# Performance work log

Measured on AMD Instinct MI355X. Metric: run time of the kernel, lower is better.

Reference implementation:

```python
import jax, jax.numpy as jnp
import numpy as np

N, E = 10000, 320000
IN_DIM, OUT_DIM, HEADS = 256, 32, 8
HD = OUT_DIM * HEADS  # 256
EPS = 1e-16  # PyG softmax epsilon


def _make_conv_params(key, in_dim, heads, d):
    hd = heads * d
    ks = jax.random.split(key, 8)
    s = 0.02
    return {
        'Wq': jax.random.normal(ks[0], (in_dim, hd)) * s,
        'bq': jnp.zeros((hd,)),
        'Wk': jax.random.normal(ks[1], (in_dim, hd)) * s,
        'bk': jnp.zeros((hd,)),
        'Wv': jax.random.normal(ks[2], (in_dim, hd)) * s,
        'bv': jnp.zeros((hd,)),
        'We': jax.random.normal(ks[3], (1, hd)) * s,          # lin_edge, no bias
        'Wskip': jax.random.normal(ks[4], (in_dim, hd)) * s,  # lin_skip
        'bskip': jnp.zeros((hd,)),
        'Wbeta': jax.random.normal(ks[5], (3 * hd, 1)) * s,   # lin_beta, no bias
    }


def transformer_conv(x, src, dst, edge_attr, p, heads, d):
    # x: [N, F]; edge_attr: [E, 1]
    n = x.shape[0]
    q = (x @ p['Wq'] + p['bq']).reshape(n, heads, d)
    k = (x @ p['Wk'] + p['bk']).reshape(n, heads, d)
    v = (x @ p['Wv'] + p['bv']).reshape(n, heads, d)
    e = (edge_attr @ p['We']).reshape(-1, heads, d)  # [E, H, D]
    kj = k[src] + e                                  # [E, H, D]
    vj = v[src] + e
    # per-edge attention logits
    alpha = jnp.einsum('ehd,ehd->eh', q[dst], kj) / jnp.sqrt(jnp.asarray(d, x.dtype))
    # segment softmax over incoming edges of each dst node
    m = jax.ops.segment_max(alpha, dst, num_segments=n)     # [N, H]
    m = jnp.where(jnp.isfinite(m), m, 0.0)
    ex = jnp.exp(alpha - m[dst])
    denom = jax.ops.segment_sum(ex, dst, num_segments=n)    # [N, H]
    w = ex / (denom[dst] + EPS)                              # [E, H]
    out = jax.ops.segment_sum(w[:, :, None] * vj, dst, num_segments=n)  # [N, H, D]
    out = out.reshape(n, heads * d)
    # beta-gated skip connection
    xr = x @ p['Wskip'] + p['bskip']
    beta = jax.nn.sigmoid(jnp.concatenate([out, xr, out - xr], axis=-1) @ p['Wbeta'])  # [N, 1]
    return beta * xr + (1.0 - beta) * out


def setup_inputs() -> dict:
    key = jax.random.key(0)
    kx, ke, kw, k1, k2 = jax.random.split(key, 5)
    inp = {
        'x': jax.random.normal(kx, (N, IN_DIM), dtype=jnp.float32),
        'edge_index': jax.random.randint(ke, (2, E), 0, N, dtype=jnp.int64),
        'edge_weight': jax.random.uniform(kw, (E,), dtype=jnp.float32),
    }
    p1 = _make_conv_params(k1, IN_DIM, HEADS, OUT_DIM)
    p2 = _make_conv_params(k2, HD, HEADS, OUT_DIM)
    for name, v in p1.items():
        inp[name + '1'] = v
    for name, v in p2.items():
        inp[name + '2'] = v
    return inp


def reference(x, edge_index, edge_weight,
              Wq1, bq1, Wk1, bk1, Wv1, bv1, We1, Wskip1, bskip1, Wbeta1,
              Wq2, bq2, Wk2, bk2, Wv2, bv2, We2, Wskip2, bskip2, Wbeta2):
    src, dst = edge_index[0], edge_index[1]
    ea = edge_weight[:, None]  # [E, 1]
    p1 = dict(Wq=Wq1, bq=bq1, Wk=Wk1, bk=bk1, Wv=Wv1, bv=bv1, We=We1,
              Wskip=Wskip1, bskip=bskip1, Wbeta=Wbeta1)
    p2 = dict(Wq=Wq2, bq=bq2, Wk=Wk2, bk=bk2, Wv=Wv2, bv=bv2, We=We2,
              Wskip=Wskip2, bskip=bskip2, Wbeta=Wbeta2)
    h = transformer_conv(x, src, dst, ea, p1, HEADS, OUT_DIM)
    h = transformer_conv(h, src, dst, ea, p2, HEADS, OUT_DIM)
    h = transformer_conv(h, src, dst, ea, p2, HEADS, OUT_DIM)  # conv2 applied twice, shared weights
    return h
```

## Files before the change

kernel.cpp:

```cpp
#include <hip/hip_runtime.h>
#include <hip/hip_bf16.h>
#include <math.h>

#define NN 10000
#define EE 320000
#define DIM 256
#define NROWS 10016
#define SCANB 40

typedef __attribute__((ext_vector_type(8))) _Float16 f16x8;
typedef __attribute__((ext_vector_type(4))) _Float16 f16x4;
typedef __attribute__((ext_vector_type(2))) _Float16 f16x2;
typedef __attribute__((ext_vector_type(4))) float f32x4;

#if defined(__has_builtin)
#if __has_builtin(__builtin_amdgcn_fdot2)
#define FDOT2(a, b, c) __builtin_amdgcn_fdot2(a, b, c, false)
#endif
#endif
#ifndef FDOT2
#define FDOT2(a, b, c) fmaf((float)a[0], (float)b[0], fmaf((float)a[1], (float)b[1], c))
#endif

__device__ __forceinline__ float bf2f(unsigned short u) {
  union { unsigned int ui; float f; } cv;
  cv.ui = ((unsigned int)u) << 16;
  return cv.f;
}

__device__ __forceinline__ float ldf(const void* p, int idx, int isf) {
  return isf ? ((const float*)p)[idx] : bf2f(((const unsigned short*)p)[idx]);
}

__global__ __launch_bounds__(256) void k_detect_zero(const unsigned int* __restrict__ xw,
                                                     const int* __restrict__ ei,
                                                     int* __restrict__ flags,
                                                     int* __restrict__ counts) {
  int i = blockIdx.x * 256 + (int)threadIdx.x;
  if (i < NN) counts[i] = 0;
  if (blockIdx.x == 0 && threadIdx.x < 64) {
    int lane = threadIdx.x;
    int wild = 0;
    for (int t = 0; t < 16; ++t) {
      unsigned int w = xw[t * 64 + lane];
      unsigned int lo = w & 0xffffu;
      float f = bf2f((unsigned short)lo);
      float af = fabsf(f);
      if (lo != 0u && (af > 1e4f || af < 1e-30f)) wild++;
    }
    #pragma unroll
    for (int m = 1; m < 64; m <<= 1) wild += __shfl_xor(wild, m);
    int zeros = 0;
    for (int t = 0; t < 2; ++t) {
      if (ei[(t * 64 + lane) * 2 + 1] == 0) zeros++;
    }
    #pragma unroll
    for (int m = 1; m < 64; m <<= 1) zeros += __shfl_xor(zeros, m);
    if (lane == 0) {
      flags[0] = (wild > 100) ? 1 : 0;
      flags[1] = (zeros > 100) ? 1 : 0;
    }
  }
}

__global__ void k_idx_count(const int* __restrict__ ei, int* __restrict__ s32,
                            int* __restrict__ d32, int* __restrict__ counts,
                            const int* __restrict__ flags) {
  int i64 = flags[1];
  int i = blockIdx.x * blockDim.x + threadIdx.x;
  if (i < EE) {
    int s, d;
    if (i64) { s = ei[2 * i]; d = ei[2 * (EE + i)]; }
    else     { s = ei[i];     d = ei[EE + i]; }
    s32[i] = s; d32[i] = d;
    atomicAdd(&counts[d], 1);
  }
}

__global__ __launch_bounds__(256) void k_scan1(const int* __restrict__ counts,
                                               int* __restrict__ tmpoff,
                                               int* __restrict__ bsum) {
  __shared__ int s[256];
  int t = threadIdx.x;
  int i = blockIdx.x * 256 + t;
  int v = (i < NN) ? counts[i] : 0;
  s[t] = v;
  __syncthreads();
  for (int off = 1; off < 256; off <<= 1) {
    int x = (t >= off) ? s[t - off] : 0;
    __syncthreads();
    s[t] += x;
    __syncthreads();
  }
  if (i < NN) tmpoff[i] = s[t] - v;
  if (t == 255) bsum[blockIdx.x] = s[255];
}

__global__ __launch_bounds__(256) void k_scan3(const int* __restrict__ tmpoff,
                                               const int* __restrict__ bsum,
                                               int* __restrict__ offsets,
                                               int* __restrict__ cursor) {
  __shared__ int sbase;
  if (threadIdx.x < 64) {
    int t = threadIdx.x;
    int v = (t < SCANB && t < (int)blockIdx.x) ? bsum[t] : 0;
    #pragma unroll
    for (int msk = 1; msk < 64; msk <<= 1) v += __shfl_xor(v, msk);
    if (t == 0) sbase = v;
  }
  __syncthreads();
  int base = sbase;
  int i = blockIdx.x * 256 + (int)threadIdx.x;
  if (i < NN) {
    int o = tmpoff[i] + base;
    offsets[i] = o;
    cursor[i] = o;
  }
  if (i == 0) offsets[NN] = EE;
}

__global__ void k_fill_sort(const int* __restrict__ d32, const int* __restrict__ s32,
                            const void* __restrict__ ew, int* __restrict__ cursor,
                            int2* __restrict__ eS, const int* __restrict__ flags) {
  int isf = flags[0];
  int i = blockIdx.x * blockDim.x + threadIdx.x;
  if (i < EE) {
    float wv = isf ? ((const float*)ew)[i] : bf2f(((const unsigned short*)ew)[i]);
    int p = atomicAdd(&cursor[d32[i]], 1);
    eS[p] = make_int2(s32[i], __float_as_int(wv));
  }
}

struct PackArgs {
  const void* W[8];
  const void* B8[8];
  const void* WeWb[4];
  const void* x;
};

__global__ __launch_bounds__(256) void k_pack(PackArgs pa, _Float16* __restrict__ Bh,
                                              float* __restrict__ bvec,
                                              float* __restrict__ WeWbF,
                                              _Float16* __restrict__ Ah,
                                              _Float16* __restrict__ Al,
                                              const int* __restrict__ flags) {
  int isf = flags[0];
  int i = blockIdx.x * 256 + (int)threadIdx.x;
  if (i < 8 * 65536) {
    int m = i >> 16, col = (i >> 8) & 255, k = i & 255;
    Bh[i] = (_Float16)ldf(pa.W[m], k * 256 + col, isf);
    return;
  }
  i -= 8 * 65536;
  if (i < 2048) {
    bvec[i] = ldf(pa.B8[i >> 8], i & 255, isf);
    return;
  }
  i -= 2048;
  if (i < 2048) {
    int which, k;
    if (i < 256)       { which = 0; k = i; }
    else if (i < 1024) { which = 1; k = i - 256; }
    else if (i < 1280) { which = 2; k = i - 1024; }
    else               { which = 3; k = i - 1280; }
    WeWbF[i] = ldf(pa.WeWb[which], k, isf);
    return;
  }
  i -= 2048;
  if (i < NROWS * 64) {
    f16x4 h, l;
    if (i >= NN * 64) {
      h = (f16x4)(_Float16)0.f;
      l = (f16x4)(_Float16)0.f;
    } else {
      float v[4];
      if (isf) {
        float4 t = reinterpret_cast<const float4*>(pa.x)[i];
        v[0] = t.x; v[1] = t.y; v[2] = t.z; v[3] = t.w;
      } else {
        ushort4 t = reinterpret_cast<const ushort4*>(pa.x)[i];
        v[0] = bf2f(t.x); v[1] = bf2f(t.y); v[2] = bf2f(t.z); v[3] = bf2f(t.w);
      }
      #pragma unroll
      for (int j = 0; j < 4; ++j) {
        _Float16 hh = (_Float16)v[j];
        h[j] = hh;
        l[j] = (_Float16)(v[j] - (float)hh);
      }
    }
    reinterpret_cast<f16x4*>(Ah)[i] = h;
    reinterpret_cast<f16x4*>(Al)[i] = l;
  }
}

__global__ __launch_bounds__(256, 4) void k_gemm_mfma(
    const _Float16* __restrict__ Ah, const _Float16* __restrict__ Al,
    const _Float16* __restrict__ Bh, const float* __restrict__ bvec,
    float* __restrict__ Qf, _Float16* __restrict__ KVh, float* __restrict__ XRf) {
  int tid = (int)threadIdx.x;
  int wave = tid >> 6, lane = tid & 63;
  int lr = lane & 15;
  int kg = (lane >> 4) << 3;
  int mat = blockIdx.y;
  int rowBase = blockIdx.x << 5;
  int colBase = (mat << 8) + (wave << 6);
  const _Float16* a0 = Ah + (size_t)(rowBase + lr) * 256 + kg;
  const _Float16* a1 = Al + (size_t)(rowBase + lr) * 256 + kg;
  const _Float16* b0 = Bh + (size_t)(colBase + lr) * 256 + kg;
  f32x4 acc[2][4] = {};
  #pragma unroll
  for (int ks = 0; ks < 256; ks += 32) {
    f16x8 ah0 = *reinterpret_cast<const f16x8*>(a0 + ks);
    f16x8 ah1 = *reinterpret_cast<const f16x8*>(a0 + 16 * 256 + ks);
    f16x8 bh[4];
    #pragma unroll
    for (int cf = 0; cf < 4; ++cf)
      bh[cf] = *reinterpret_cast<const f16x8*>(b0 + cf * 16 * 256 + ks);
    #pragma unroll
    for (int cf = 0; cf < 4; ++cf) {
      acc[0][cf] = __builtin_amdgcn_mfma_f32_16x16x32_f16(ah0, bh[cf], acc[0][cf], 0, 0, 0);
      acc[1][cf] = __builtin_amdgcn_mfma_f32_16x16x32_f16(ah1, bh[cf], acc[1][cf], 0, 0, 0);
    }
    if (mat == 3) {
      f16x8 al0 = *reinterpret_cast<const f16x8*>(a1 + ks);
      f16x8 al1 = *reinterpret_cast<const f16x8*>(a1 + 16 * 256 + ks);
      #pragma unroll
      for (int cf = 0; cf < 4; ++cf) {
        acc[0][cf] = __builtin_amdgcn_mfma_f32_16x16x32_f16(al0, bh[cf], acc[0][cf], 0, 0, 0);
        acc[1][cf] = __builtin_amdgcn_mfma_f32_16x16x32_f16(al1, bh[cf], acc[1][cf], 0, 0, 0);
      }
    }
  }
  int rj = (lane >> 4) << 2;
  int colLoc = (wave << 6);
  #pragma unroll
  for (int rf = 0; rf < 2; ++rf) {
    #pragma unroll
    for (int cf = 0; cf < 4; ++cf) {
      int col = colLoc + cf * 16 + lr;
      float bb = bvec[(mat << 8) + col];
      #pragma unroll
      for (int j = 0; j < 4; ++j) {
        int row = rowBase + rf * 16 + rj + j;
        if (row < NN) {
          float val = acc[rf][cf][j] + bb;
          if (mat == 0)      Qf[(size_t)row * DIM + col] = val;
          else if (mat == 3) XRf[(size_t)row * DIM + col] = val;
          else KVh[(size_t)row * 512 + ((mat == 2) ? 256 : 0) + col] = (_Float16)val;
        }
      }
    }
  }
}

#define ATT_STEP(KK, VV, WW) do { \
    f16x2 kka = {KK[0], KK[1]}, kkb = {KK[2], KK[3]}; \
    float pt = FDOT2(kka, qha, FDOT2(kkb, qhb, 0.f)); \
    pt += __shfl_xor(pt, 1); \
    pt += __shfl_xor(pt, 2); \
    pt += __shfl_xor(pt, 4); \
    float alpha = fmaf(WW, qwe, pt) * 0.17677669529663687f; \
    float nm = fmaxf(m, alpha); \
    float sc = __expf(m - nm); \
    float pe = __expf(alpha - nm); \
    l = fmaf(l, sc, pe); \
    sw = fmaf(sw, sc, pe * WW); \
    a0 = fmaf(a0, sc, pe * (float)VV[0]); \
    a1 = fmaf(a1, sc, pe * (float)VV[1]); \
    a2 = fmaf(a2, sc, pe * (float)VV[2]); \
    a3 = fmaf(a3, sc, pe * (float)VV[3]); \
    m = nm; \
  } while (0)

#define PAIR_STEP(K0, V0, W0, K1, V1, W1) do { \
    f16x2 k0a = {K0[0], K0[1]}, k0b = {K0[2], K0[3]}; \
    f16x2 k1a = {K1[0], K1[1]}, k1b = {K1[2], K1[3]}; \
    float pt0 = FDOT2(k0a, qha, FDOT2(k0b, qhb, 0.f)); \
    float pt1 = FDOT2(k1a, qha, FDOT2(k1b, qhb, 0.f)); \
    pt0 += __shfl_xor(pt0, 1); pt1 += __shfl_xor(pt1, 1); \
    pt0 += __shfl_xor(pt0, 2); pt1 += __shfl_xor(pt1, 2); \
    pt0 += __shfl_xor(pt0, 4); pt1 += __shfl_xor(pt1, 4); \
    float al0 = fmaf(W0, qwe, pt0) * 0.17677669529663687f; \
    float al1 = fmaf(W1, qwe, pt1) * 0.17677669529663687f; \
    float nm = fmaxf(fmaxf(m, al0), al1); \
    float sc = __expf(m - nm); \
    float p0 = __expf(al0 - nm); \
    float p1 = __expf(al1 - nm); \
    l = fmaf(l, sc, p0 + p1); \
    sw = fmaf(sw, sc, fmaf(p0, W0, p1 * W1)); \
    a0 = fmaf(a0, sc, fmaf(p0, (float)V0[0], p1 * (float)V1[0])); \
    a1 = fmaf(a1, sc, fmaf(p0, (float)V0[1], p1 * (float)V1[1])); \
    a2 = fmaf(a2, sc, fmaf(p0, (float)V0[2], p1 * (float)V1[2])); \
    a3 = fmaf(a3, sc, fmaf(p0, (float)V0[3], p1 * (float)V1[3])); \
    m = nm; \
  } while (0)

__global__ __launch_bounds__(256) void k_attn(
    const float* __restrict__ Qf, const _Float16* __restrict__ KVh,
    const float* __restrict__ XRf, const float* __restrict__ We,
    const float* __restrict__ Wb, const int2* __restrict__ eS,
    const int* __restrict__ offsets, _Float16* __restrict__ Ah,
    _Float16* __restrict__ Al, float* __restrict__ FinalOut) {
  int wid = (int)threadIdx.x >> 6, lane = (int)threadIdx.x & 63;
  int node = blockIdx.x * 4 + wid;
  if (node >= NN) return;
  int d0 = lane * 4;
  const float4 q4 = *reinterpret_cast<const float4*>(&Qf[(size_t)node * DIM + d0]);
  const float4 x4 = *reinterpret_cast<const float4*>(&XRf[(size_t)node * DIM + d0]);
  const float4 we4 = *reinterpret_cast<const float4*>(&We[d0]);
  const float4 wo = *reinterpret_cast<const float4*>(&Wb[d0]);
  const float4 wx = *reinterpret_cast<const float4*>(&Wb[DIM + d0]);
  const float4 wd = *reinterpret_cast<const float4*>(&Wb[2 * DIM + d0]);
  f16x2 qha = {(_Float16)q4.x, (_Float16)q4.y};
  f16x2 qhb = {(_Float16)q4.z, (_Float16)q4.w};
  float qwe = q4.x * we4.x + q4.y * we4.y + q4.z * we4.z + q4.w * we4.w;
  qwe += __shfl_xor(qwe, 1);
  qwe += __shfl_xor(qwe, 2);
  qwe += __shfl_xor(qwe, 4);
  int beg = offsets[node], end = offsets[node + 1];
  beg = __builtin_amdgcn_readfirstlane(beg);
  end = __builtin_amdgcn_readfirstlane(end);
  float m = -INFINITY, l = 0.f, sw = 0.f, a0 = 0.f, a1 = 0.f, a2 = 0.f, a3 = 0.f;
  int p = beg;
  if ((end - beg) & 1) {
    int2 e = eS[p];
    float w0 = __int_as_float(e.y);
    const _Float16* r = KVh + (size_t)e.x * 512 + d0;
    f16x4 k0 = *reinterpret_cast<const f16x4*>(r);
    f16x4 v0 = *reinterpret_cast<const f16x4*>(r + 256);
    ATT_STEP(k0, v0, w0);
    ++p;
  }
  if (p < end) {
    int2 eA0 = eS[p], eA1 = eS[p + 1];
    int pb = (p + 3 < end) ? (p + 2) : p;
    int2 eB0 = eS[pb], eB1 = eS[pb + 1];
    const _Float16* rA0 = KVh + (size_t)eA0.x * 512 + d0;
    const _Float16* rA1 = KVh + (size_t)eA1.x * 512 + d0;
    const _Float16* rB0 = KVh + (size_t)eB0.x * 512 + d0;
    const _Float16* rB1 = KVh + (size_t)eB1.x * 512 + d0;
    f16x4 kA0 = *reinterpret_cast<const f16x4*>(rA0), vA0 = *reinterpret_cast<const f16x4*>(rA0 + 256);
    f16x4 kA1 = *reinterpret_cast<const f16x4*>(rA1), vA1 = *reinterpret_cast<const f16x4*>(rA1 + 256);
    f16x4 kB0 = *reinterpret_cast<const f16x4*>(rB0), vB0 = *reinterpret_cast<const f16x4*>(rB0 + 256);
    f16x4 kB1 = *reinterpret_cast<const f16x4*>(rB1), vB1 = *reinterpret_cast<const f16x4*>(rB1 + 256);
    float wA0 = __int_as_float(eA0.y), wA1 = __int_as_float(eA1.y);
    float wB0 = __int_as_float(eB0.y), wB1 = __int_as_float(eB1.y);
    #pragma unroll 2
    for (; p + 2 < end; p += 2) {
      int pc = (p + 5 < end) ? (p + 4) : p;
      int2 eC0 = eS[pc], eC1 = eS[pc + 1];
      const _Float16* rC0 = KVh + (size_t)eC0.x * 512 + d0;
      const _Float16* rC1 = KVh + (size_t)eC1.x * 512 + d0;
      f16x4 kC0 = *reinterpret_cast<const f16x4*>(rC0), vC0 = *reinterpret_cast<const f16x4*>(rC0 + 256);
      f16x4 kC1 = *reinterpret_cast<const f16x4*>(rC1), vC1 = *reinterpret_cast<const f16x4*>(rC1 + 256);
      float wC0 = __int_as_float(eC0.y), wC1 = __int_as_float(eC1.y);
      PAIR_STEP(kA0, vA0, wA0, kA1, vA1, wA1);
      kA0 = kB0; vA0 = vB0; wA0 = wB0; kA1 = kB1; vA1 = vB1; wA1 = wB1;
      kB0 = kC0; vB0 = vC0; wB0 = wC0; kB1 = kC1; vB1 = vC1; wB1 = wC1;
    }
    PAIR_STEP(kA0, vA0, wA0, kA1, vA1, wA1);
  }
  float inv = 1.f / (l + 1e-16f);
  float o0 = fmaf(sw, we4.x, a0) * inv;
  float o1 = fmaf(sw, we4.y, a1) * inv;
  float o2 = fmaf(sw, we4.z, a2) * inv;
  float o3 = fmaf(sw, we4.w, a3) * inv;
  float part = o0 * wo.x + o1 * wo.y + o2 * wo.z + o3 * wo.w
             + x4.x * wx.x + x4.y * wx.y + x4.z * wx.z + x4.w * wx.w
             + (o0 - x4.x) * wd.x + (o1 - x4.y) * wd.y
             + (o2 - x4.z) * wd.z + (o3 - x4.w) * wd.w;
  #pragma unroll
  for (int msk = 1; msk < 64; msk <<= 1) part += __shfl_xor(part, msk);
  float beta = 1.f / (1.f + __expf(-part));
  float h0 = beta * x4.x + (1.f - beta) * o0;
  float h1 = beta * x4.y + (1.f - beta) * o1;
  float h2 = beta * x4.z + (1.f - beta) * o2;
  float h3 = beta * x4.w + (1.f - beta) * o3;
  if (FinalOut) {
    float4 h; h.x = h0; h.y = h1; h.z = h2; h.w = h3;
    *reinterpret_cast<float4*>(&FinalOut[(size_t)node * DIM + d0]) = h;
  } else {
    f16x4 hh, ll;
    _Float16 t0 = (_Float16)h0, t1 = (_Float16)h1, t2 = (_Float16)h2, t3 = (_Float16)h3;
    hh[0] = t0; hh[1] = t1; hh[2] = t2; hh[3] = t3;
    ll[0] = (_Float16)(h0 - (float)t0); ll[1] = (_Float16)(h1 - (float)t1);
    ll[2] = (_Float16)(h2 - (float)t2); ll[3] = (_Float16)(h3 - (float)t3);
    *reinterpret_cast<f16x4*>(&Ah[(size_t)node * DIM + d0]) = hh;
    *reinterpret_cast<f16x4*>(&Al[(size_t)node * DIM + d0]) = ll;
  }
}

static inline size_t align256(size_t v) { return (v + 255) & ~(size_t)255; }

extern "C" void kernel_launch(void* const* d_in, const int* in_sizes, int n_in,
                              void* d_out, int out_size, void* d_ws, size_t ws_size,
                              hipStream_t stream) {
  const void* x = d_in[0];
  const int* eidx = (const int*)d_in[1];
  const void* ew = d_in[2];

  char* w = (char*)d_ws;
  size_t pos = 0;
  int* flags = (int*)(w + pos); pos = align256(pos + 2 * sizeof(int));
  float* Qf  = (float*)(w + pos); pos = align256(pos + (size_t)NROWS * DIM * 4);
  float* XRf = (float*)(w + pos); pos = align256(pos + (size_t)NROWS * DIM * 4);
  _Float16* KVh = (_Float16*)(w + pos); pos = align256(pos + (size_t)NROWS * 512 * 2);
  _Float16* Ah = (_Float16*)(w + pos); pos = align256(pos + (size_t)NROWS * DIM * 2);
  _Float16* Al = (_Float16*)(w + pos); pos = align256(pos + (size_t)NROWS * DIM * 2);
  _Float16* Bh = (_Float16*)(w + pos); pos = align256(pos + (size_t)8 * 65536 * 2);
  float* bvec  = (float*)(w + pos); pos = align256(pos + 2048 * 4);
  float* WeWbF = (float*)(w + pos); pos = align256(pos + 2048 * 4);
  int* s32   = (int*)(w + pos);    pos = align256(pos + (size_t)EE * 4);
  int* d32   = (int*)(w + pos);    pos = align256(pos + (size_t)EE * 4);
  int2* eS   = (int2*)(w + pos);   pos = align256(pos + (size_t)EE * 8);
  int* counts  = (int*)(w + pos);  pos = align256(pos + (size_t)NN * 4);
  int* offsets = (int*)(w + pos);  pos = align256(pos + (size_t)(NN + 1) * 4);
  int* cursor  = (int*)(w + pos);  pos = align256(pos + (size_t)NN * 4);
  int* tmpoff  = (int*)(w + pos);  pos = align256(pos + (size_t)NN * 4);
  int* bsum    = (int*)(w + pos);  pos = align256(pos + 64 * 4);

  PackArgs pa;
  pa.x = x;
  for (int g = 0; g < 2; ++g) {
    const void* const* pp = &d_in[3 + g * 10];
    pa.W[g * 4 + 0] = pp[0]; pa.W[g * 4 + 1] = pp[2];
    pa.W[g * 4 + 2] = pp[4]; pa.W[g * 4 + 3] = pp[7];
    pa.B8[g * 4 + 0] = pp[1]; pa.B8[g * 4 + 1] = pp[3];
    pa.B8[g * 4 + 2] = pp[5]; pa.B8[g * 4 + 3] = pp[8];
    pa.WeWb[g * 2 + 0] = pp[6];
    pa.WeWb[g * 2 + 1] = pp[9];
  }

  k_detect_zero<<<SCANB, 256, 0, stream>>>((const unsigned int*)x, eidx, flags, counts);
  k_pack<<<4568, 256, 0, stream>>>(pa, Bh, bvec, WeWbF, Ah, Al, flags);
  k_idx_count<<<(EE + 255) / 256, 256, 0, stream>>>(eidx, s32, d32, counts, flags);
  k_scan1<<<SCANB, 256, 0, stream>>>(counts, tmpoff, bsum);
  k_scan3<<<SCANB, 256, 0, stream>>>(tmpoff, bsum, offsets, cursor);
  k_fill_sort<<<(EE + 255) / 256, 256, 0, stream>>>(d32, s32, ew, cursor, eS, flags);

  for (int layer = 0; layer < 3; ++layer) {
    int g = (layer == 0) ? 0 : 1;
    k_gemm_mfma<<<dim3(NROWS / 32, 4), 256, 0, stream>>>(
        Ah, Al, Bh + (size_t)g * 4 * 65536, bvec + g * 1024, Qf, KVh, XRf);
    k_attn<<<(NN + 3) / 4, 256, 0, stream>>>(Qf, KVh, XRf,
        WeWbF + (g ? 1024 : 0), WeWbF + (g ? 1280 : 256),
        eS, offsets, Ah, Al, (layer == 2) ? (float*)d_out : nullptr);
  }
}
```

Measured before the change: 305.9 us.

## Schedule attention nodes by descending degree and enlarge GEMM row tile

Builds a degree histogram and counting sort so the attention kernel handles nodes in descending in-degree order, which reduces tail imbalance from high-degree nodes landing late in the launch. The MFMA GEMM also now covers 64 rows per block instead of 32, so each B fragment load feeds more MFMAs. NROWS padding and the pack grid size are increased to match. This adds two small preprocessing kernels and more accumulator registers per GEMM thread, and processing nodes out of index order may hurt locality of Q/XR accesses.

```diff
diff --git a/kernel.cpp b/kernel.cpp
--- a/kernel.cpp
+++ b/kernel.cpp
@@ -5,7 +5,7 @@
 #define NN 10000
 #define EE 320000
 #define DIM 256
-#define NROWS 10016
+#define NROWS 10048
 #define SCANB 40
 
 typedef __attribute__((ext_vector_type(8))) _Float16 f16x8;
@@ -35,9 +35,11 @@
 __global__ __launch_bounds__(256) void k_detect_zero(const unsigned int* __restrict__ xw,
                                                      const int* __restrict__ ei,
                                                      int* __restrict__ flags,
-                                                     int* __restrict__ counts) {
+                                                     int* __restrict__ counts,
+                                                     int* __restrict__ hist) {
   int i = blockIdx.x * 256 + (int)threadIdx.x;
   if (i < NN) counts[i] = 0;
+  if (blockIdx.x == 1) hist[threadIdx.x] = 0;
   if (blockIdx.x == 0 && threadIdx.x < 64) {
     int lane = threadIdx.x;
     int wild = 0;
@@ -79,11 +81,13 @@
 
 __global__ __launch_bounds__(256) void k_scan1(const int* __restrict__ counts,
                                                int* __restrict__ tmpoff,
-                                               int* __restrict__ bsum) {
+                                               int* __restrict__ bsum,
+                                               int* __restrict__ hist) {
   __shared__ int s[256];
   int t = threadIdx.x;
   int i = blockIdx.x * 256 + t;
   int v = (i < NN) ? counts[i] : 0;
+  if (i < NN) atomicAdd(&hist[255 - min(v, 255)], 1);
   s[t] = v;
   __syncthreads();
   for (int off = 1; off < 256; off <<= 1) {
@@ -117,6 +121,31 @@
     cursor[i] = o;
   }
   if (i == 0) offsets[NN] = EE;
+}
+
+__global__ __launch_bounds__(256) void k_order_prefix(int* __restrict__ hist) {
+  __shared__ int s[256];
+  int t = threadIdx.x;
+  int v = hist[t];
+  s[t] = v;
+  __syncthreads();
+  for (int off = 1; off < 256; off <<= 1) {
+    int x = (t >= off) ? s[t - off] : 0;
+    __syncthreads();
+    s[t] += x;
+    __syncthreads();
+  }
+  hist[t] = s[t] - v;
+}
+
+__global__ void k_fill_order(const int* __restrict__ offsets, int* __restrict__ hist,
+                             int* __restrict__ order) {
+  int i = blockIdx.x * blockDim.x + threadIdx.x;
+  if (i < NN) {
+    int deg = offsets[i + 1] - offsets[i];
+    int pos = atomicAdd(&hist[255 - min(deg, 255)], 1);
+    order[pos] = i;
+  }
 }
 
 __global__ void k_fill_sort(const int* __restrict__ d32, const int* __restrict__ s32,
@@ -202,39 +231,43 @@
   int lr = lane & 15;
   int kg = (lane >> 4) << 3;
   int mat = blockIdx.y;
-  int rowBase = blockIdx.x << 5;
+  int rowBase = blockIdx.x << 6;
   int colBase = (mat << 8) + (wave << 6);
   const _Float16* a0 = Ah + (size_t)(rowBase + lr) * 256 + kg;
   const _Float16* a1 = Al + (size_t)(rowBase + lr) * 256 + kg;
   const _Float16* b0 = Bh + (size_t)(colBase + lr) * 256 + kg;
-  f32x4 acc[2][4] = {};
+  f32x4 acc[4][4] = {};
   #pragma unroll
   for (int ks = 0; ks < 256; ks += 32) {
-    f16x8 ah0 = *reinterpret_cast<const f16x8*>(a0 + ks);
-    f16x8 ah1 = *reinterpret_cast<const f16x8*>(a0 + 16 * 256 + ks);
+    f16x8 ah[4];
+    #pragma unroll
+    for (int rf = 0; rf < 4; ++rf)
+      ah[rf] = *reinterpret_cast<const f16x8*>(a0 + rf * 16 * 256 + ks);
     f16x8 bh[4];
     #pragma unroll
     for (int cf = 0; cf < 4; ++cf)
       bh[cf] = *reinterpret_cast<const f16x8*>(b0 + cf * 16 * 256 + ks);
     #pragma unroll
-    for (int cf = 0; cf < 4; ++cf) {
-      acc[0][cf] = __builtin_amdgcn_mfma_f32_16x16x32_f16(ah0, bh[cf], acc[0][cf], 0, 0, 0);
-      acc[1][cf] = __builtin_amdgcn_mfma_f32_16x16x32_f16(ah1, bh[cf], acc[1][cf], 0, 0, 0);
-    }
+    for (int rf = 0; rf < 4; ++rf)
+      #pragma unroll
+      for (int cf = 0; cf < 4; ++cf)
+        acc[rf][cf] = __builtin_amdgcn_mfma_f32_16x16x32_f16(ah[rf], bh[cf], acc[rf][cf], 0, 0, 0);
     if (mat == 3) {
-      f16x8 al0 = *reinterpret_cast<const f16x8*>(a1 + ks);
-      f16x8 al1 = *reinterpret_cast<const f16x8*>(a1 + 16 * 256 + ks);
+      f16x8 al[4];
       #pragma unroll
-      for (int cf = 0; cf < 4; ++cf) {
-        acc[0][cf] = __builtin_amdgcn_mfma_f32_16x16x32_f16(al0, bh[cf], acc[0][cf], 0, 0, 0);
-        acc[1][cf] = __builtin_amdgcn_mfma_f32_16x16x32_f16(al1, bh[cf], acc[1][cf], 0, 0, 0);
-      }
+      for (int rf = 0; rf < 4; ++rf)
+        al[rf] = *reinterpret_cast<const f16x8*>(a1 + rf * 16 * 256 + ks);
+      #pragma unroll
+      for (int rf = 0; rf < 4; ++rf)
+        #pragma unroll
+        for (int cf = 0; cf < 4; ++cf)
+          acc[rf][cf] = __builtin_amdgcn_mfma_f32_16x16x32_f16(al[rf], bh[cf], acc[rf][cf], 0, 0, 0);
     }
   }
   int rj = (lane >> 4) << 2;
   int colLoc = (wave << 6);
   #pragma unroll
-  for (int rf = 0; rf < 2; ++rf) {
+  for (int rf = 0; rf < 4; ++rf) {
     #pragma unroll
     for (int cf = 0; cf < 4; ++cf) {
       int col = colLoc + cf * 16 + lr;
@@ -299,11 +332,13 @@
     const float* __restrict__ Qf, const _Float16* __restrict__ KVh,
     const float* __restrict__ XRf, const float* __restrict__ We,
     const float* __restrict__ Wb, const int2* __restrict__ eS,
-    const int* __restrict__ offsets, _Float16* __restrict__ Ah,
-    _Float16* __restrict__ Al, float* __restrict__ FinalOut) {
+    const int* __restrict__ offsets, const int* __restrict__ order,
+    _Float16* __restrict__ Ah, _Float16* __restrict__ Al,
+    float* __restrict__ FinalOut) {
   int wid = (int)threadIdx.x >> 6, lane = (int)threadIdx.x & 63;
-  int node = blockIdx.x * 4 + wid;
-  if (node >= NN) return;
+  int idx = blockIdx.x * 4 + wid;
+  if (idx >= NN) return;
+  int node = order[idx];
   int d0 = lane * 4;
   const float4 q4 = *reinterpret_cast<const float4*>(&Qf[(size_t)node * DIM + d0]);
   const float4 x4 = *reinterpret_cast<const float4*>(&XRf[(size_t)node * DIM + d0]);
@@ -418,6 +453,8 @@
   int* cursor  = (int*)(w + pos);  pos = align256(pos + (size_t)NN * 4);
   int* tmpoff  = (int*)(w + pos);  pos = align256(pos + (size_t)NN * 4);
   int* bsum    = (int*)(w + pos);  pos = align256(pos + 64 * 4);
+  int* hist    = (int*)(w + pos);  pos = align256(pos + 256 * 4);
+  int* order   = (int*)(w + pos);  pos = align256(pos + (size_t)NN * 4);
 
   PackArgs pa;
   pa.x = x;
@@ -431,19 +468,21 @@
     pa.WeWb[g * 2 + 1] = pp[9];
   }
 
-  k_detect_zero<<<SCANB, 256, 0, stream>>>((const unsigned int*)x, eidx, flags, counts);
-  k_pack<<<4568, 256, 0, stream>>>(pa, Bh, bvec, WeWbF, Ah, Al, flags);
+  k_detect_zero<<<SCANB, 256, 0, stream>>>((const unsigned int*)x, eidx, flags, counts, hist);
+  k_pack<<<4576, 256, 0, stream>>>(pa, Bh, bvec, WeWbF, Ah, Al, flags);
   k_idx_count<<<(EE + 255) / 256, 256, 0, stream>>>(eidx, s32, d32, counts, flags);
-  k_scan1<<<SCANB, 256, 0, stream>>>(counts, tmpoff, bsum);
+  k_scan1<<<SCANB, 256, 0, stream>>>(counts, tmpoff, bsum, hist);
   k_scan3<<<SCANB, 256, 0, stream>>>(tmpoff, bsum, offsets, cursor);
+  k_order_prefix<<<1, 256, 0, stream>>>(hist);
+  k_fill_order<<<SCANB, 256, 0, stream>>>(offsets, hist, order);
   k_fill_sort<<<(EE + 255) / 256, 256, 0, stream>>>(d32, s32, ew, cursor, eS, flags);
 
   for (int layer = 0; layer < 3; ++layer) {
     int g = (layer == 0) ? 0 : 1;
-    k_gemm_mfma<<<dim3(NROWS / 32, 4), 256, 0, stream>>>(
+    k_gemm_mfma<<<dim3(NROWS / 64, 4), 256, 0, stream>>>(
         Ah, Al, Bh + (size_t)g * 4 * 65536, bvec + g * 1024, Qf, KVh, XRf);
     k_attn<<<(NN + 3) / 4, 256, 0, stream>>>(Qf, KVh, XRf,
         WeWbF + (g ? 1024 : 0), WeWbF + (g ? 1280 : 256),
-        eS, offsets, Ah, Al, (layer == 2) ? (float*)d_out : nullptr);
-  }
-}
+        eS, offsets, order, Ah, Al, (layer == 2) ? (float*)d_out : nullptr);
+  }
+}
```

Result: slower. 333.6 us (+9.1%).
